# Performance work log

Hardware: AMD Instinct MI355X
Metric: run time of the kernel (lower is better)

Reference implementation:

```python
import jax, jax.numpy as jnp
import numpy as np

EPS = 1e-5

def _ste(x, q):
    # straight-through estimator: forward = q, backward = identity
    return x + jax.lax.stop_gradient(q - x)

def quant_act_int4(x):
    # per-token absmax quantization to int4 range [-8, 7] (dequantized)
    s = jnp.clip(jnp.max(jnp.abs(x), axis=-1, keepdims=True), EPS, None) / 7.0
    q = jnp.clip(jnp.round(x / s), -8.0, 7.0) * s
    return _ste(x, q)

def ternary_weight(w):
    # absmean ternary quantization: scale = mean(|w|), w_q in {-1,0,+1} * scale
    scale = jnp.clip(jnp.mean(jnp.abs(w)), EPS, None)
    t = jnp.clip(jnp.round(w / scale), -1.0, 1.0)
    return _ste(w, t * scale)

def setup_inputs() -> dict:
    key = jax.random.key(0)
    kx, kw = jax.random.split(key)
    in_features, out_features = 4096, 16384
    x = jax.random.normal(kx, (4, 2048, in_features), dtype=jnp.float32)
    # kaiming_uniform_(a=sqrt(5)) -> U(-b, b), b = sqrt(6/((1+5)*fan_in)) = 1/sqrt(fan_in)
    bound = 1.0 / np.sqrt(in_features)
    latent_weight = jax.random.uniform(kw, (out_features, in_features), dtype=jnp.float32,
                                       minval=-bound, maxval=bound)
    return {"x": x, "latent_weight": latent_weight}

def reference(x, latent_weight):
    xq = quant_act_int4(x)                    # (B, S, in)
    w_eff = ternary_weight(latent_weight)     # (out, in)
    return jnp.einsum('bsi,oi->bso', xq, w_eff)
```

## Files before the change

kernel.cpp:

```cpp
#include <hip/hip_runtime.h>
#include <stdint.h>


#define K_DIM 4096
#define M_DIM 8192
#define N_DIM 16384

typedef int v4i __attribute__((ext_vector_type(4)));

typedef __attribute__((address_space(1))) void gvoid_t;
typedef __attribute__((address_space(3))) void lvoid_t;

__device__ __forceinline__ void gl_lds16(const void* g, void* l) {
    __builtin_amdgcn_global_load_lds((gvoid_t*)(void*)g, (lvoid_t*)l, 16, 0, 0);
}

__global__ __launch_bounds__(256) void wabs_partial_k(const float* __restrict__ w,
                                                      double* __restrict__ part) {
    const long n4 = (long)N_DIM * K_DIM / 4;
    long i = (long)blockIdx.x * blockDim.x + threadIdx.x;
    const long stride = (long)gridDim.x * blockDim.x;
    const float4* w4 = (const float4*)w;
    double s = 0.0;
    for (; i < n4; i += stride) {
        float4 v = w4[i];
        s += (double)fabsf(v.x);
        s += (double)fabsf(v.y);
        s += (double)fabsf(v.z);
        s += (double)fabsf(v.w);
    }
    __shared__ double red[256];
    const int tid = threadIdx.x;
    red[tid] = s;
    __syncthreads();
    for (int w2 = 128; w2 > 0; w2 >>= 1) {
        if (tid < w2) red[tid] += red[tid + w2];
        __syncthreads();
    }
    if (tid == 0) part[blockIdx.x] = red[0];
}

__global__ __launch_bounds__(256) void wscale_final_k(const double* __restrict__ part,
                                                      float* __restrict__ wscale) {
    __shared__ double red[256];
    const int tid = threadIdx.x;
    double s = 0.0;
    for (int i = tid; i < 1024; i += 256) s += part[i];
    red[tid] = s;
    __syncthreads();
    for (int w2 = 128; w2 > 0; w2 >>= 1) {
        if (tid < w2) red[tid] += red[tid + w2];
        __syncthreads();
    }
    if (tid == 0) {
        double mean = red[0] / (double)((long)N_DIM * K_DIM);
        *wscale = fmaxf((float)mean, 1e-5f);
    }
}

__global__ __launch_bounds__(256) void wquant_k(const float* __restrict__ w,
                                                signed char* __restrict__ qw,
                                                const float* __restrict__ wscale) {
    const float sc = *wscale;
    const long n4 = (long)N_DIM * K_DIM / 4;
    long i = (long)blockIdx.x * blockDim.x + threadIdx.x;
    const long stride = (long)gridDim.x * blockDim.x;
    const float4* w4 = (const float4*)w;
    int* q4 = (int*)qw;
    for (; i < n4; i += stride) {
        float4 v = w4[i];
        union { signed char c[4]; int u; } p;
        p.c[0] = (signed char)fminf(fmaxf(rintf(v.x / sc), -1.f), 1.f);
        p.c[1] = (signed char)fminf(fmaxf(rintf(v.y / sc), -1.f), 1.f);
        p.c[2] = (signed char)fminf(fmaxf(rintf(v.z / sc), -1.f), 1.f);
        p.c[3] = (signed char)fminf(fmaxf(rintf(v.w / sc), -1.f), 1.f);
        q4[i] = p.u;
    }
}

__global__ __launch_bounds__(256) void xquant_k(const float* __restrict__ x,
                                                signed char* __restrict__ qx,
                                                float* __restrict__ sx,
                                                const float* __restrict__ wscale) {
    const int row = blockIdx.x;
    const int tid = threadIdx.x;
    const float4* xr = (const float4*)(x + (long)row * K_DIM);
    float4 v[4];
    float am = 0.f;
#pragma unroll
    for (int j = 0; j < 4; ++j) {
        v[j] = xr[tid + j * 256];
        am = fmaxf(am, fmaxf(fmaxf(fabsf(v[j].x), fabsf(v[j].y)),
                             fmaxf(fabsf(v[j].z), fabsf(v[j].w))));
    }
#pragma unroll
    for (int off = 32; off > 0; off >>= 1) am = fmaxf(am, __shfl_down(am, off));
    __shared__ float wm[4];
    if ((tid & 63) == 0) wm[tid >> 6] = am;
    __syncthreads();
    am = fmaxf(fmaxf(wm[0], wm[1]), fmaxf(wm[2], wm[3]));
    const float s = fmaxf(am, 1e-5f) / 7.0f;
    int* qr = (int*)(qx + (long)row * K_DIM);
#pragma unroll
    for (int j = 0; j < 4; ++j) {
        union { signed char c[4]; int u; } p;
        p.c[0] = (signed char)fminf(fmaxf(rintf(v[j].x / s), -8.f), 7.f);
        p.c[1] = (signed char)fminf(fmaxf(rintf(v[j].y / s), -8.f), 7.f);
        p.c[2] = (signed char)fminf(fmaxf(rintf(v[j].z / s), -8.f), 7.f);
        p.c[3] = (signed char)fminf(fmaxf(rintf(v[j].w / s), -8.f), 7.f);
        qr[tid + j * 256] = p.u;
    }
    if (tid == 0) sx[row] = s * (*wscale);
}

__global__ __launch_bounds__(512, 2) void gemm_k(const signed char* __restrict__ qx,
                                                 const signed char* __restrict__ qw,
                                                 const float* __restrict__ sx,
                                                 float* __restrict__ out) {
    __shared__ __align__(16) signed char lds[4][32768];

    const int tid  = threadIdx.x;
    const int lane = tid & 63;
    const int wave = tid >> 6;
    const int wm = wave >> 2;
    const int wn = wave & 3;

    const int bid = blockIdx.x;
    const int xcd = bid & 7;
    const int cid = bid >> 3;
    const int mt  = (cid >> 1) & 31;
    const int nt  = (xcd << 3) + ((cid >> 6) << 1) + (cid & 1);
    const int m0 = mt << 8;
    const int n0 = nt << 8;

    const int r = tid >> 2;
    const int g = ((tid & 3) - ((tid >> 3) & 3)) & 3;
    const signed char* gA = qx + (long)(m0 + r) * K_DIM + (g << 4);
    const signed char* gB = qw + (long)(n0 + r) * K_DIM + (g << 4);
    const int oSA0 = tid << 4;
    const int oSA1 = (tid << 4) + 8192;
    const int oSB0 = (tid << 4) + 16384;
    const int oSB1 = (tid << 4) + 24576;

    const int fr = lane & 15;
    const int fq = lane >> 4;
    int offA[8], offB[4];
#pragma unroll
    for (int i = 0; i < 8; ++i) {
        const int ra = wm * 128 + i * 16 + fr;
        offA[i] = ra * 64 + (((fq + (ra >> 1)) & 3) << 4);
    }
#pragma unroll
    for (int j = 0; j < 4; ++j) {
        const int rb = wn * 64 + j * 16 + fr;
        offB[j] = 16384 + rb * 64 + (((fq + (rb >> 1)) & 3) << 4);
    }

    v4i acc[8][4];
#pragma unroll
    for (int i = 0; i < 8; ++i)
#pragma unroll
        for (int j = 0; j < 4; ++j) acc[i][j] = 0;

    gl_lds16(gA,                      &lds[0][oSA0]);
    gl_lds16(gA + 128 * K_DIM,        &lds[0][oSA1]);
    gl_lds16(gB,                      &lds[0][oSB0]);
    gl_lds16(gB + 128 * K_DIM,        &lds[0][oSB1]);
    gl_lds16(gA + 64,                 &lds[1][oSA0]);
    gl_lds16(gA + 128 * K_DIM + 64,   &lds[1][oSA1]);
    gl_lds16(gB + 64,                 &lds[1][oSB0]);
    gl_lds16(gB + 128 * K_DIM + 64,   &lds[1][oSB1]);

    for (int t = 0; t < 64; ++t) {
        if (t == 63) { asm volatile("s_waitcnt vmcnt(0)" ::: "memory"); }
        else         { asm volatile("s_waitcnt vmcnt(4)" ::: "memory"); }
        __builtin_amdgcn_s_barrier();

        const signed char* cur = lds[t & 3];
        signed char* nb = (signed char*)lds[(t + 2) & 3];

        if (t < 62) {
            const long k2 = (long)(t + 2) << 6;
            gl_lds16(gA + k2,                 nb + oSA0);
            gl_lds16(gA + 128 * K_DIM + k2,   nb + oSA1);
            gl_lds16(gB + k2,                 nb + oSB0);
            gl_lds16(gB + 128 * K_DIM + k2,   nb + oSB1);
        }

        v4i a[8], b[4];
#pragma unroll
        for (int j = 0; j < 4; ++j) b[j] = *(const v4i*)(cur + offB[j]);
#pragma unroll
        for (int i = 0; i < 8; ++i) a[i] = *(const v4i*)(cur + offA[i]);

        __builtin_amdgcn_s_setprio(1);
#pragma unroll
        for (int i = 0; i < 8; ++i)
#pragma unroll
            for (int j = 0; j < 4; ++j)
                acc[i][j] = __builtin_amdgcn_mfma_i32_16x16x64_i8(a[i], b[j], acc[i][j], 0, 0, 0);
        __builtin_amdgcn_s_setprio(0);
    }

#pragma unroll
    for (int i = 0; i < 8; ++i) {
        const int mrow = m0 + wm * 128 + i * 16 + fq * 4;
#pragma unroll
        for (int rr = 0; rr < 4; ++rr) {
            const int m = mrow + rr;
            const float sm = sx[m];
            float* orow = out + (long)m * N_DIM + n0 + wn * 64 + fr;
#pragma unroll
            for (int j = 0; j < 4; ++j)
                orow[j * 16] = (float)acc[i][j][rr] * sm;
        }
    }
}

extern "C" void kernel_launch(void* const* d_in, const int* in_sizes, int n_in,
                              void* d_out, int out_size, void* d_ws, size_t ws_size,
                              hipStream_t stream) {
    const float* x = (const float*)d_in[0];
    const float* w = (const float*)d_in[1];
    float* out = (float*)d_out;
    char* ws = (char*)d_ws;

    double* part         = (double*)(ws);
    float*  wscale       = (float*)(ws + 8192);
    float*  sx           = (float*)(ws + 16384);
    signed char* qx      = (signed char*)(ws + 65536);
    signed char* qw      = (signed char*)(ws + 65536 + (size_t)33554432);

    wabs_partial_k<<<1024, 256, 0, stream>>>(w, part);
    wscale_final_k<<<1, 256, 0, stream>>>(part, wscale);
    wquant_k<<<2048, 256, 0, stream>>>(w, qw, wscale);
    xquant_k<<<8192, 256, 0, stream>>>(x, qx, sx, wscale);
    gemm_k<<<2048, 512, 0, stream>>>(qx, qw, sx, out);
}
```

Before: 1.278 ms.

## Prefetch next LDS fragments into registers and deepen global prefetch to three stages

Restructures the int8 MFMA GEMM main loop so that each iteration loads the next k-step's A/B fragments from LDS into a second register set while the MFMAs run on the current set (register double buffering). The global-to-LDS prefetch distance grows from two to three of the four LDS buffers. Per-fragment offset arrays are collapsed into a base offset plus constant strides. This is meant to hide LDS read latency behind MFMA issue, at the cost of roughly doubling fragment registers, which puts occupancy at launch_bounds(512,2) at risk.

```diff
diff --git a/kernel.cpp b/kernel.cpp
--- a/kernel.cpp
+++ b/kernel.cpp
@@ -113,6 +113,39 @@
     if (tid == 0) sx[row] = s * (*wscale);
 }
 
+
+#define GEMM_BODY(T, CA, CB, NA, NB)                                          \
+    {                                                                         \
+        if ((T) < 62) { asm volatile("s_waitcnt vmcnt(4)" ::: "memory"); }    \
+        else          { asm volatile("s_waitcnt vmcnt(0)" ::: "memory"); }    \
+        asm volatile("s_barrier" ::: "memory");                               \
+        if ((T) < 63) {                                                       \
+            const signed char* nxt = &lds[((T) + 1) & 3][0];                  \
+            _Pragma("unroll")                                                 \
+            for (int j_ = 0; j_ < 4; ++j_)                                    \
+                NB[j_] = *(const v4i*)(nxt + offB0 + j_ * 1024);              \
+            _Pragma("unroll")                                                 \
+            for (int i_ = 0; i_ < 8; ++i_)                                    \
+                NA[i_] = *(const v4i*)(nxt + offA0 + i_ * 1024);              \
+        }                                                                     \
+        if ((T) <= 60) {                                                      \
+            signed char* sb = &lds[((T) + 3) & 3][0];                         \
+            const long k3 = (long)((T) + 3) << 6;                             \
+            gl_lds16(gA + k3,                 sb + oSA0);                     \
+            gl_lds16(gA + 128 * K_DIM + k3,   sb + oSA1);                     \
+            gl_lds16(gB + k3,                 sb + oSB0);                     \
+            gl_lds16(gB + 128 * K_DIM + k3,   sb + oSB1);                     \
+        }                                                                     \
+        __builtin_amdgcn_s_setprio(1);                                        \
+        _Pragma("unroll")                                                     \
+        for (int i_ = 0; i_ < 8; ++i_)                                        \
+            _Pragma("unroll")                                                 \
+            for (int j_ = 0; j_ < 4; ++j_)                                    \
+                acc[i_][j_] = __builtin_amdgcn_mfma_i32_16x16x64_i8(          \
+                    CA[i_], CB[j_], acc[i_][j_], 0, 0, 0);                    \
+        __builtin_amdgcn_s_setprio(0);                                        \
+    }
+
 __global__ __launch_bounds__(512, 2) void gemm_k(const signed char* __restrict__ qx,
                                                  const signed char* __restrict__ qw,
                                                  const float* __restrict__ sx,
@@ -144,17 +177,9 @@
 
     const int fr = lane & 15;
     const int fq = lane >> 4;
-    int offA[8], offB[4];
-#pragma unroll
-    for (int i = 0; i < 8; ++i) {
-        const int ra = wm * 128 + i * 16 + fr;
-        offA[i] = ra * 64 + (((fq + (ra >> 1)) & 3) << 4);
-    }
-#pragma unroll
-    for (int j = 0; j < 4; ++j) {
-        const int rb = wn * 64 + j * 16 + fr;
-        offB[j] = 16384 + rb * 64 + (((fq + (rb >> 1)) & 3) << 4);
-    }
+    const int slot = ((fq + (fr >> 1)) & 3) << 4;
+    const int offA0 = (wm * 128 + fr) * 64 + slot;
+    const int offB0 = 16384 + (wn * 64 + fr) * 64 + slot;
 
     v4i acc[8][4];
 #pragma unroll
@@ -162,44 +187,32 @@
 #pragma unroll
         for (int j = 0; j < 4; ++j) acc[i][j] = 0;
 
-    gl_lds16(gA,                      &lds[0][oSA0]);
-    gl_lds16(gA + 128 * K_DIM,        &lds[0][oSA1]);
-    gl_lds16(gB,                      &lds[0][oSB0]);
-    gl_lds16(gB + 128 * K_DIM,        &lds[0][oSB1]);
-    gl_lds16(gA + 64,                 &lds[1][oSA0]);
-    gl_lds16(gA + 128 * K_DIM + 64,   &lds[1][oSA1]);
-    gl_lds16(gB + 64,                 &lds[1][oSB0]);
-    gl_lds16(gB + 128 * K_DIM + 64,   &lds[1][oSB1]);
-
-    for (int t = 0; t < 64; ++t) {
-        if (t == 63) { asm volatile("s_waitcnt vmcnt(0)" ::: "memory"); }
-        else         { asm volatile("s_waitcnt vmcnt(4)" ::: "memory"); }
-        __builtin_amdgcn_s_barrier();
-
-        const signed char* cur = lds[t & 3];
-        signed char* nb = (signed char*)lds[(t + 2) & 3];
-
-        if (t < 62) {
-            const long k2 = (long)(t + 2) << 6;
-            gl_lds16(gA + k2,                 nb + oSA0);
-            gl_lds16(gA + 128 * K_DIM + k2,   nb + oSA1);
-            gl_lds16(gB + k2,                 nb + oSB0);
-            gl_lds16(gB + 128 * K_DIM + k2,   nb + oSB1);
-        }
-
-        v4i a[8], b[4];
-#pragma unroll
-        for (int j = 0; j < 4; ++j) b[j] = *(const v4i*)(cur + offB[j]);
-#pragma unroll
-        for (int i = 0; i < 8; ++i) a[i] = *(const v4i*)(cur + offA[i]);
-
-        __builtin_amdgcn_s_setprio(1);
-#pragma unroll
-        for (int i = 0; i < 8; ++i)
-#pragma unroll
-            for (int j = 0; j < 4; ++j)
-                acc[i][j] = __builtin_amdgcn_mfma_i32_16x16x64_i8(a[i], b[j], acc[i][j], 0, 0, 0);
-        __builtin_amdgcn_s_setprio(0);
+    gl_lds16(gA,                       &lds[0][oSA0]);
+    gl_lds16(gA + 128 * K_DIM,         &lds[0][oSA1]);
+    gl_lds16(gB,                       &lds[0][oSB0]);
+    gl_lds16(gB + 128 * K_DIM,         &lds[0][oSB1]);
+    gl_lds16(gA + 64,                  &lds[1][oSA0]);
+    gl_lds16(gA + 128 * K_DIM + 64,    &lds[1][oSA1]);
+    gl_lds16(gB + 64,                  &lds[1][oSB0]);
+    gl_lds16(gB + 128 * K_DIM + 64,    &lds[1][oSB1]);
+    gl_lds16(gA + 128,                 &lds[2][oSA0]);
+    gl_lds16(gA + 128 * K_DIM + 128,   &lds[2][oSA1]);
+    gl_lds16(gB + 128,                 &lds[2][oSB0]);
+    gl_lds16(gB + 128 * K_DIM + 128,   &lds[2][oSB1]);
+
+    asm volatile("s_waitcnt vmcnt(8)" ::: "memory");
+    asm volatile("s_barrier" ::: "memory");
+
+    v4i a0[8], b0[4], a1[8], b1[4];
+#pragma unroll
+    for (int j = 0; j < 4; ++j) b0[j] = *(const v4i*)(&lds[0][0] + offB0 + j * 1024);
+#pragma unroll
+    for (int i = 0; i < 8; ++i) a0[i] = *(const v4i*)(&lds[0][0] + offA0 + i * 1024);
+
+#pragma unroll 1
+    for (int t = 0; t < 64; t += 2) {
+        GEMM_BODY(t,     a0, b0, a1, b1);
+        GEMM_BODY(t + 1, a1, b1, a0, b0);
     }
 
 #pragma unroll
```

Result: no change. 1.276 ms (-0.1%).
